# Optimization experiments

Measured on AMD Instinct MI355X. Metric: run time of the kernel, lower is better.

Reference implementation:

```python
import jax, jax.numpy as jnp
import numpy as np

N_EVENTS = 16384   # original pixel events
D = 128            # input_size
H = 128            # hidden_size
K = 9              # kernel 3x3 -> patch coords
S = 2048           # number of patch sequences
LMAX = 108         # max sequence length
T = 147456         # total patch events = sum(lengths) = 9 * N_EVENTS


def setup_inputs() -> dict:
    key = jax.random.key(0)
    ks = jax.random.split(key, 8)
    events = jax.random.normal(ks[0], (N_EVENTS, D), jnp.float32)
    pos_id = jax.random.randint(ks[1], (T,), 0, K, dtype=jnp.int32)
    orig_event_idx = jax.random.randint(ks[2], (T,), 0, N_EVENTS, dtype=jnp.int32)
    # alternating 36/108 lengths: 1024*36 + 1024*108 = 147456 = T
    lengths = jnp.where(jnp.arange(S) % 2 == 0, 36, 108).astype(jnp.int32)
    std = float(np.sqrt(2.0 / (D + H)))
    scatter_w = jax.random.normal(ks[3], (K, H, D), jnp.float32) * std
    gather_w = jax.random.normal(ks[4], (K, H, H), jnp.float32) * std
    lstm_std = float(1.0 / np.sqrt(H))
    w_ih = jax.random.uniform(ks[5], (4 * H, H), jnp.float32, -lstm_std, lstm_std)
    w_hh = jax.random.uniform(ks[6], (4 * H, H), jnp.float32, -lstm_std, lstm_std)
    ln_g = jnp.ones((H,), jnp.float32)
    ln_b = jnp.zeros((H,), jnp.float32)
    return dict(events=events, scatter_w=scatter_w, gather_w=gather_w,
                w_ih=w_ih, w_hh=w_hh, ln_g=ln_g, ln_b=ln_b,
                pos_id=pos_id, orig_event_idx=orig_event_idx, lengths=lengths)


def _pos_proj(x, W, pos_id):
    # position-indexed projection: out[t] = W[pos_id[t]] @ x[t]
    # loop over small fixed K=9 with masked accumulate (matches the torch loop)
    out = jnp.zeros((x.shape[0], W.shape[1]), x.dtype)
    for k in range(W.shape[0]):
        out = out + jnp.where((pos_id == k)[:, None], x @ W[k].T, 0.0)
    return out


def reference(events, scatter_w, gather_w, w_ih, w_hh, ln_g, ln_b,
              pos_id, orig_event_idx, lengths):
    # scatter events to patch replicas
    x = events[orig_event_idx]                           # [T, D]
    x = _pos_proj(x, scatter_w, pos_id)                  # [T, H]

    # flat (sequence-major) -> padded [S, LMAX, H]
    seq_offsets = jnp.cumsum(lengths) - lengths          # [S]
    seq_ids = jnp.repeat(jnp.arange(S), lengths, total_repeat_length=T)
    pos_in_seq = jnp.arange(T) - seq_offsets[seq_ids]
    padded = jnp.zeros((S, LMAX, H), x.dtype).at[seq_ids, pos_in_seq].set(x)

    # single-layer bias-free LSTM (pytorch gate order i, f, g, o), zero init.
    # zero-padding after each sequence's valid region leaves valid outputs
    # identical to a PackedSequence LSTM.
    def step(carry, xt):                                 # xt: [S, H]
        h, c = carry
        gates = xt @ w_ih.T + h @ w_hh.T                 # [S, 4H]
        i, f, g, o = jnp.split(gates, 4, axis=-1)
        c = jax.nn.sigmoid(f) * c + jax.nn.sigmoid(i) * jnp.tanh(g)
        h = jax.nn.sigmoid(o) * jnp.tanh(c)
        return (h, c), h

    init = (jnp.zeros((S, H), x.dtype), jnp.zeros((S, H), x.dtype))
    _, hs = jax.lax.scan(step, init, jnp.swapaxes(padded, 0, 1))  # [LMAX, S, H]
    o_flat = jnp.swapaxes(hs, 0, 1)[seq_ids, pos_in_seq]          # [T, H]

    o_flat = _pos_proj(o_flat, gather_w, pos_id)                  # [T, H]

    # gather patch events back to pixel events (scatter-add) + residual + LN
    out = jnp.zeros((N_EVENTS, H), x.dtype).at[orig_event_idx].add(o_flat)
    out = out + events                                   # input_proj is None (D == H)
    mu = jnp.mean(out, axis=-1, keepdims=True)
    var = jnp.var(out, axis=-1, keepdims=True)
    out = (out - mu) * jax.lax.rsqrt(var + 1e-5) * ln_g + ln_b
    return out
```

## Files before the change

kernel.cpp:

```cpp
#include <hip/hip_runtime.h>

#define N_EVENTS 16384
#define DIM 128
#define NK 9
#define NSEQ 2048
#define TT 147456
#define CHUNK 64
#define NCHUNK_MAX (TT/CHUNK + NK)
#define NHBLK 576

typedef __attribute__((ext_vector_type(8))) short bf16x8;
typedef __attribute__((ext_vector_type(4))) float f32x4;
typedef __attribute__((ext_vector_type(4))) int i32x4;

#define OFF_EV     0UL
#define OFF_WC     (OFF_EV   + (size_t)N_EVENTS*DIM*2)
#define OFF_SCAT   (OFF_WC   + (size_t)512*256*2)
#define OFF_GATH   (OFF_SCAT + (size_t)NK*DIM*DIM*2)
#define OFF_XS     (OFF_GATH + (size_t)NK*DIM*DIM*2)
#define OFF_HS     (OFF_XS   + (size_t)TT*DIM*2)
#define OFF_KLIST  (OFF_HS   + (size_t)TT*DIM*2)
#define OFF_ACC    (OFF_KLIST+ (size_t)TT*4)
#define OFF_SEQOFF (OFF_ACC  + (size_t)N_EVENTS*DIM*4)
#define OFF_GROUP  (OFF_SEQOFF + (size_t)NSEQ*4)
#define OFF_MISC   (OFF_GROUP  + (size_t)NSEQ*4)
#define OFF_BH     (OFF_MISC   + 256UL)

__device__ __forceinline__ short f2b(float f) {
    union { float f; unsigned u; } v; v.f = f;
    unsigned r = (v.u + 0x7FFFu + ((v.u >> 16) & 1u)) >> 16;
    return (short)r;
}

__global__ void convert_kernel(const float* __restrict__ ev, const float* __restrict__ wih,
                               const float* __restrict__ whh, const float* __restrict__ sw,
                               const float* __restrict__ gw,
                               short* __restrict__ evb, short* __restrict__ wcb,
                               short* __restrict__ swb, short* __restrict__ gwb,
                               float* __restrict__ acc) {
    int idx = blockIdx.x * blockDim.x + threadIdx.x;
    if (idx < N_EVENTS * DIM) { evb[idx] = f2b(ev[idx]); acc[idx] = 0.f; }
    if (idx < 512 * DIM) {
        int j = idx >> 7, d = idx & 127;
        wcb[j * 256 + d]       = f2b(wih[idx]);
        wcb[j * 256 + 128 + d] = f2b(whh[idx]);
    }
    if (idx < NK * DIM * DIM) { swb[idx] = f2b(sw[idx]); gwb[idx] = f2b(gw[idx]); }
}

__global__ void hist_kernel(const int* __restrict__ pos, int* __restrict__ blockhist) {
    __shared__ int h[NK];
    int tid = threadIdx.x;
    if (tid < NK) h[tid] = 0;
    __syncthreads();
    atomicAdd(&h[pos[blockIdx.x * 256 + tid]], 1);
    __syncthreads();
    if (tid < NK) blockhist[blockIdx.x * NK + tid] = h[tid];
}

__global__ void scan_kernel(int* __restrict__ blockhist, int* __restrict__ misc) {
    __shared__ int h[NHBLK * NK];
    int tid = threadIdx.x;
    for (int i = tid; i < NHBLK * NK; i += 256) h[i] = blockhist[i];
    __syncthreads();
    if (tid < NK) {
        int run = 0;
        for (int b = 0; b < NHBLK; b++) {
            int v = h[b * NK + tid];
            h[b * NK + tid] = run;
            run += v;
        }
        misc[tid] = run;
    }
    __syncthreads();
    if (tid == 0) {
        int ko = 0, co = 0;
        for (int k = 0; k < NK; k++) {
            int c = misc[k];
            misc[32 + k] = ko;
            misc[48 + k] = co;
            ko += c;
            co += (c + CHUNK - 1) / CHUNK;
        }
        misc[48 + NK] = co;
    }
    __syncthreads();
    for (int i = tid; i < NHBLK * NK; i += 256) blockhist[i] = h[i];
}

__global__ void setup_kernel(const int* __restrict__ lengths,
                             int* __restrict__ seq_off, int* __restrict__ grouped) {
    __shared__ int lens[NSEQ];
    __shared__ int tsum[256], tlong[256];
    int tid = threadIdx.x;
    for (int i = tid; i < NSEQ; i += 256) lens[i] = lengths[i];
    __syncthreads();
    int base = tid * 8;
    int ls[8]; int s = 0, lc = 0;
    #pragma unroll
    for (int i = 0; i < 8; i++) { ls[i] = lens[base + i]; s += ls[i]; lc += (ls[i] > 64) ? 1 : 0; }
    tsum[tid] = s; tlong[tid] = lc;
    __syncthreads();
    for (int d = 1; d < 256; d <<= 1) {
        int a = (tid >= d) ? tsum[tid - d] : 0;
        int b = (tid >= d) ? tlong[tid - d] : 0;
        __syncthreads();
        tsum[tid] += a; tlong[tid] += b;
        __syncthreads();
    }
    int nlong_total = tlong[255];
    int excl = tsum[tid] - s;
    int excl_long = tlong[tid] - lc;
    int run = 0, runl = 0;
    #pragma unroll
    for (int i = 0; i < 8; i++) {
        int sid = base + i;
        seq_off[sid] = excl + run;
        int longs_before = excl_long + runl;
        if (ls[i] > 64) { grouped[longs_before] = sid; runl++; }
        else            { grouped[nlong_total + (sid - longs_before)] = sid; }
        run += ls[i];
    }
}

__global__ void fill2_kernel(const int* __restrict__ pos, const int* __restrict__ blockhist,
                             const int* __restrict__ misc, int* __restrict__ klist) {
    __shared__ int off[NK];
    int tid = threadIdx.x;
    if (tid < NK) off[tid] = misc[32 + tid] + blockhist[blockIdx.x * NK + tid];
    __syncthreads();
    int t = blockIdx.x * 256 + tid;
    int p = atomicAdd(&off[pos[t]], 1);
    klist[p] = t;
}

__global__ void bucket_gemm(const short* __restrict__ src, const short* __restrict__ wall,
                            const int* __restrict__ klist, const int* __restrict__ misc,
                            const int* __restrict__ orig, short* __restrict__ xs_out,
                            float* __restrict__ acc, int mode) {
    const int* chunkoff = misc + 48;
    int b = blockIdx.x;
    if (b >= chunkoff[NK]) return;
    int k = 0;
    while (k < NK - 1 && chunkoff[k + 1] <= b) k++;
    int lc = b - chunkoff[k];
    int cnt = misc[k];
    int base = misc[32 + k] + lc * CHUNK;
    int nv = min(CHUNK, cnt - lc * CHUNK);

    __shared__ int tok[CHUNK], dst[CHUNK];
    __shared__ short A[CHUNK * 136];
    int tid = threadIdx.x;
    if (tid < CHUNK) {
        int tv = klist[base + ((tid < nv) ? tid : 0)];
        tok[tid] = tv;
        dst[tid] = orig[tv];
    }
    __syncthreads();
    {
        int row = tid >> 2, part = tid & 3;
        int ridx = (mode == 0) ? dst[row] : tok[row];
        const i32x4* s4 = (const i32x4*)(src + (size_t)ridx * DIM + part * 32);
        i32x4* d4 = (i32x4*)(A + row * 136 + part * 32);
        d4[0] = s4[0]; d4[1] = s4[1]; d4[2] = s4[2]; d4[3] = s4[3];
    }
    __syncthreads();
    int wave = tid >> 6, lane = tid & 63, l15 = lane & 15, q = lane >> 4;
    const short* wk = wall + (size_t)k * DIM * DIM;
    bf16x8 Bf[2][4];
    #pragma unroll
    for (int nt = 0; nt < 2; nt++) {
        int h = wave * 32 + nt * 16 + l15;
        #pragma unroll
        for (int kt = 0; kt < 4; kt++)
            Bf[nt][kt] = *(const bf16x8*)(wk + h * DIM + kt * 32 + q * 8);
    }
    f32x4 C[4][2];
    #pragma unroll
    for (int mt = 0; mt < 4; mt++)
        #pragma unroll
        for (int nt = 0; nt < 2; nt++) C[mt][nt] = (f32x4){0.f, 0.f, 0.f, 0.f};
    #pragma unroll
    for (int mt = 0; mt < 4; mt++) {
        bf16x8 Afr[4];
        const short* ar = A + (mt * 16 + l15) * 136 + q * 8;
        Afr[0] = *(const bf16x8*)(ar);
        Afr[1] = *(const bf16x8*)(ar + 32);
        Afr[2] = *(const bf16x8*)(ar + 64);
        Afr[3] = *(const bf16x8*)(ar + 96);
        #pragma unroll
        for (int nt = 0; nt < 2; nt++)
            #pragma unroll
            for (int kt = 0; kt < 4; kt++)
                C[mt][nt] = __builtin_amdgcn_mfma_f32_16x16x32_bf16(Afr[kt], Bf[nt][kt], C[mt][nt], 0, 0, 0);
    }
    if (mode == 0) {
        __syncthreads();
        #pragma unroll
        for (int mt = 0; mt < 4; mt++)
            #pragma unroll
            for (int nt = 0; nt < 2; nt++)
                #pragma unroll
                for (int r = 0; r < 4; r++) {
                    int row = mt * 16 + q * 4 + r;
                    int col = wave * 32 + nt * 16 + l15;
                    A[row * 136 + col] = f2b(C[mt][nt][r]);
                }
        __syncthreads();
        int row = tid >> 2, part = tid & 3;
        if (row < nv) {
            const i32x4* s4 = (const i32x4*)(A + row * 136 + part * 32);
            i32x4* d4 = (i32x4*)(xs_out + (size_t)tok[row] * DIM + part * 32);
            d4[0] = s4[0]; d4[1] = s4[1]; d4[2] = s4[2]; d4[3] = s4[3];
        }
    } else {
        #pragma unroll
        for (int mt = 0; mt < 4; mt++)
            #pragma unroll
            for (int nt = 0; nt < 2; nt++)
                #pragma unroll
                for (int r = 0; r < 4; r++) {
                    int row = mt * 16 + q * 4 + r;
                    if (row < nv) {
                        int col = wave * 32 + nt * 16 + l15;
                        atomicAdd(acc + (size_t)dst[row] * DIM + col, C[mt][nt][r]);
                    }
                }
    }
}

#define MF(a, b, c) __builtin_amdgcn_mfma_f32_16x16x32_bf16(a, b, c, 0, 0, 0)

#define LSTM_STEP(J, PF) { \
    const int i_ = ib8 + (J); \
    f32x4 Cxi = {0.f,0.f,0.f,0.f}, Cxf = {0.f,0.f,0.f,0.f}; \
    f32x4 Cxg = {0.f,0.f,0.f,0.f}, Cxo = {0.f,0.f,0.f,0.f}; \
    Cxi = MF(PF[0], Bf[0][0], Cxi); Cxf = MF(PF[0], Bf[1][0], Cxf); \
    Cxg = MF(PF[0], Bf[2][0], Cxg); Cxo = MF(PF[0], Bf[3][0], Cxo); \
    Cxi = MF(PF[1], Bf[0][1], Cxi); Cxf = MF(PF[1], Bf[1][1], Cxf); \
    Cxg = MF(PF[1], Bf[2][1], Cxg); Cxo = MF(PF[1], Bf[3][1], Cxo); \
    Cxi = MF(PF[2], Bf[0][2], Cxi); Cxf = MF(PF[2], Bf[1][2], Cxf); \
    Cxg = MF(PF[2], Bf[2][2], Cxg); Cxo = MF(PF[2], Bf[3][2], Cxo); \
    Cxi = MF(PF[3], Bf[0][3], Cxi); Cxf = MF(PF[3], Bf[1][3], Cxf); \
    Cxg = MF(PF[3], Bf[2][3], Cxg); Cxo = MF(PF[3], Bf[3][3], Cxo); \
    bf16x8 Hf0, Hf1, Hf2, Hf3; \
    { const short* hp_ = hb + (((J) + 7) & 7) * 1088 + l15 * 136 + ql * 8; \
      Hf0 = *(const bf16x8*)(hp_);      Hf1 = *(const bf16x8*)(hp_ + 32); \
      Hf2 = *(const bf16x8*)(hp_ + 64); Hf3 = *(const bf16x8*)(hp_ + 96); } \
    f32x4 Chi = {0.f,0.f,0.f,0.f}, Chf = {0.f,0.f,0.f,0.f}; \
    f32x4 Chg = {0.f,0.f,0.f,0.f}, Cho = {0.f,0.f,0.f,0.f}; \
    Chi = MF(Hf0, Bf[0][4], Chi); Chf = MF(Hf0, Bf[1][4], Chf); \
    Chg = MF(Hf0, Bf[2][4], Chg); Cho = MF(Hf0, Bf[3][4], Cho); \
    Chi = MF(Hf1, Bf[0][5], Chi); Chf = MF(Hf1, Bf[1][5], Chf); \
    Chg = MF(Hf1, Bf[2][5], Chg); Cho = MF(Hf1, Bf[3][5], Cho); \
    Chi = MF(Hf2, Bf[0][6], Chi); Chf = MF(Hf2, Bf[1][6], Chf); \
    Chg = MF(Hf2, Bf[2][6], Chg); Cho = MF(Hf2, Bf[3][6], Cho); \
    Chi = MF(Hf3, Bf[0][7], Chi); Chf = MF(Hf3, Bf[1][7], Chf); \
    Chg = MF(Hf3, Bf[2][7], Chg); Cho = MF(Hf3, Bf[3][7], Cho); \
    if (l15 < 8) { \
        const short* xp_ = xs + xoff; \
        PF[0] = *(const bf16x8*)(xp_);      PF[1] = *(const bf16x8*)(xp_ + 32); \
        PF[2] = *(const bf16x8*)(xp_ + 64); PF[3] = *(const bf16x8*)(xp_ + 96); \
    } \
    xoff += ((i_ + 4) <= my_len) ? DIM : 0; \
    f32x4 Gi = Cxi + Chi, Gf = Cxf + Chf, Gg = Cxg + Chg, Go = Cxo + Cho; \
    { \
        int src_ = lane & 31; \
        float i2 = __shfl(Gi[2], src_, 64), i3 = __shfl(Gi[3], src_, 64); \
        float f2 = __shfl(Gf[2], src_, 64), f3 = __shfl(Gf[3], src_, 64); \
        float g2 = __shfl(Gg[2], src_, 64), g3 = __shfl(Gg[3], src_, 64); \
        float o2 = __shfl(Go[2], src_, 64), o3 = __shfl(Go[3], src_, 64); \
        float iA = lo ? Gi[0] : i2, iB = lo ? Gi[1] : i3; \
        float fA = lo ? Gf[0] : f2, fB = lo ? Gf[1] : f3; \
        float gA = lo ? Gg[0] : g2, gB = lo ? Gg[1] : g3; \
        float oA = lo ? Go[0] : o2, oB = lo ? Go[1] : o3; \
        if (i_ < lenA) { \
            float si = 1.f / (1.f + __expf(-iA)); \
            float sf = 1.f / (1.f + __expf(-fA)); \
            float so = 1.f / (1.f + __expf(-oA)); \
            float tg = 1.f - 2.f / (__expf(2.f * gA) + 1.f); \
            float cn = sf * cA + si * tg; \
            float th = 1.f - 2.f / (__expf(2.f * cn) + 1.f); \
            cA = cn; \
            hb[(J) * 1088 + rowA * 136 + u] = f2b(so * th); \
        } \
        if (i_ < lenB) { \
            float si = 1.f / (1.f + __expf(-iB)); \
            float sf = 1.f / (1.f + __expf(-fB)); \
            float so = 1.f / (1.f + __expf(-oB)); \
            float tg = 1.f - 2.f / (__expf(2.f * gB) + 1.f); \
            float cn = sf * cB + si * tg; \
            float th = 1.f - 2.f / (__expf(2.f * cn) + 1.f); \
            cB = cn; \
            hb[(J) * 1088 + rowB * 136 + u] = f2b(so * th); \
        } \
    } \
    __syncthreads(); \
}

__global__ __launch_bounds__(512, 2) void lstm_kernel(
        const short* __restrict__ xs, const short* __restrict__ wc,
        short* __restrict__ hstore, const int* __restrict__ seq_off,
        const int* __restrict__ grouped, const int* __restrict__ lengths) {
    __shared__ int s_off[8], s_len[8];
    __shared__ short hchunk[11][8][136];
    int tid = threadIdx.x;
    if (tid < 8) {
        int s = grouped[blockIdx.x * 8 + tid];
        s_off[tid] = seq_off[s];
        s_len[tid] = lengths[s];
    }
    for (int j = tid; j < 11 * 8 * 136; j += 512) ((short*)hchunk)[j] = 0;
    __syncthreads();
    int lane = tid & 63, l15 = lane & 15, ql = lane >> 4;
    int wave = tid >> 6;
    int u = wave * 16 + l15;
    short* hb = (short*)hchunk;
    bf16x8 Bf[4][8];
    #pragma unroll
    for (int g = 0; g < 4; g++) {
        int j = g * 128 + u;
        #pragma unroll
        for (int kt = 0; kt < 8; kt++)
            Bf[g][kt] = *(const bf16x8*)(wc + j * 256 + kt * 32 + ql * 8);
    }
    int maxlen = 0;
    #pragma unroll
    for (int i = 0; i < 8; i++) maxlen = max(maxlen, s_len[i]);
    int my_off = (l15 < 8) ? s_off[l15] : 0;
    int my_len = (l15 < 8) ? s_len[l15] : 1;
    bool lo = (ql < 2);
    int rowA = lo ? (ql * 4 + 0) : ((ql - 2) * 4 + 2);
    int rowB = lo ? (ql * 4 + 1) : ((ql - 2) * 4 + 3);
    int lenA = s_len[rowA], lenB = s_len[rowB];
    float cA = 0.f, cB = 0.f;
    bf16x8 Pf0[4], Pf1[4];
    #pragma unroll
    for (int k = 0; k < 4; k++) { Pf0[k] = (bf16x8){0,0,0,0,0,0,0,0}; Pf1[k] = Pf0[k]; }
    int xoff = my_off * DIM + ql * 8;
    if (l15 < 8) {
        const short* xp = xs + xoff;
        Pf0[0] = *(const bf16x8*)(xp);      Pf0[1] = *(const bf16x8*)(xp + 32);
        Pf0[2] = *(const bf16x8*)(xp + 64); Pf0[3] = *(const bf16x8*)(xp + 96);
    }
    int xoff1 = xoff + ((my_len > 1) ? DIM : 0);
    if (l15 < 8) {
        const short* xp = xs + xoff1;
        Pf1[0] = *(const bf16x8*)(xp);      Pf1[1] = *(const bf16x8*)(xp + 32);
        Pf1[2] = *(const bf16x8*)(xp + 64); Pf1[3] = *(const bf16x8*)(xp + 96);
    }
    xoff = xoff1 + ((my_len > 2) ? DIM : 0);

    int nb8 = (maxlen + 7) >> 3;
    for (int ob = 0; ob < nb8; ob++) {
        int ib8 = ob * 8;
        LSTM_STEP(0, Pf0)
        LSTM_STEP(1, Pf1)
        LSTM_STEP(2, Pf0)
        LSTM_STEP(3, Pf1)
        LSTM_STEP(4, Pf0)
        LSTM_STEP(5, Pf1)
        LSTM_STEP(6, Pf0)
        LSTM_STEP(7, Pf1)
        #pragma unroll
        for (int it = 0; it < 2; it++) {
            int idx = tid + it * 512;
            int st = idx >> 7, s = (idx >> 4) & 7, part = idx & 15;
            int ig = ib8 + st;
            if (ig < s_len[s]) {
                i32x4 v = *(const i32x4*)&hchunk[st][s][part * 8];
                *(i32x4*)(hstore + (size_t)(s_off[s] + ig) * DIM + part * 8) = v;
            }
        }
        __syncthreads();
    }
}

__global__ void ln_kernel(const float* __restrict__ acc, const float* __restrict__ events,
                          const float* __restrict__ g, const float* __restrict__ bta,
                          float* __restrict__ out) {
    int tid = threadIdx.x;
    int wave = tid >> 6, lane = tid & 63;
    int e = blockIdx.x * 4 + wave;
    const float2* a2 = (const float2*)(acc + (size_t)e * DIM);
    const float2* e2 = (const float2*)(events + (size_t)e * DIM);
    float2 av = a2[lane], ev = e2[lane];
    float x0 = av.x + ev.x, x1 = av.y + ev.y;
    float sm = x0 + x1, sq = x0 * x0 + x1 * x1;
    #pragma unroll
    for (int m = 1; m < 64; m <<= 1) {
        sm += __shfl_xor(sm, m, 64);
        sq += __shfl_xor(sq, m, 64);
    }
    float mean = sm * (1.f / DIM);
    float var = sq * (1.f / DIM) - mean * mean;
    float rs = rsqrtf(var + 1e-5f);
    float2 gv = ((const float2*)g)[lane], bv = ((const float2*)bta)[lane];
    float2 ov;
    ov.x = (x0 - mean) * rs * gv.x + bv.x;
    ov.y = (x1 - mean) * rs * gv.y + bv.y;
    ((float2*)(out + (size_t)e * DIM))[lane] = ov;
}

extern "C" void kernel_launch(void* const* d_in, const int* in_sizes, int n_in,
                              void* d_out, int out_size, void* d_ws, size_t ws_size,
                              hipStream_t stream) {
    const float* events = (const float*)d_in[0];
    const float* scat   = (const float*)d_in[1];
    const float* gath   = (const float*)d_in[2];
    const float* wih    = (const float*)d_in[3];
    const float* whh    = (const float*)d_in[4];
    const float* lng    = (const float*)d_in[5];
    const float* lnb    = (const float*)d_in[6];
    const int* posid    = (const int*)d_in[7];
    const int* orig     = (const int*)d_in[8];
    const int* lens     = (const int*)d_in[9];
    char* ws = (char*)d_ws;
    short* evb   = (short*)(ws + OFF_EV);
    short* wcb   = (short*)(ws + OFF_WC);
    short* swb   = (short*)(ws + OFF_SCAT);
    short* gwb   = (short*)(ws + OFF_GATH);
    short* xs    = (short*)(ws + OFF_XS);
    short* hs    = (short*)(ws + OFF_HS);
    int*   klist = (int*)(ws + OFF_KLIST);
    float* acc   = (float*)(ws + OFF_ACC);
    int*   seqo  = (int*)(ws + OFF_SEQOFF);
    int*   grp   = (int*)(ws + OFF_GROUP);
    int*   misc  = (int*)(ws + OFF_MISC);
    int*   bh    = (int*)(ws + OFF_BH);
    float* out   = (float*)d_out;

    convert_kernel<<<8192, 256, 0, stream>>>(events, wih, whh, scat, gath, evb, wcb, swb, gwb, acc);
    hist_kernel<<<NHBLK, 256, 0, stream>>>(posid, bh);
    scan_kernel<<<1, 256, 0, stream>>>(bh, misc);
    setup_kernel<<<1, 256, 0, stream>>>(lens, seqo, grp);
    fill2_kernel<<<NHBLK, 256, 0, stream>>>(posid, bh, misc, klist);
    bucket_gemm<<<NCHUNK_MAX, 256, 0, stream>>>(evb, swb, klist, misc, orig, xs, nullptr, 0);
    lstm_kernel<<<256, 512, 0, stream>>>(xs, wcb, hs, seqo, grp, lens);
    bucket_gemm<<<NCHUNK_MAX, 256, 0, stream>>>(hs, gwb, klist, misc, orig, nullptr, acc, 1);
    ln_kernel<<<4096, 256, 0, stream>>>(acc, events, lng, lnb, out);
}
```

Baseline: 347.3 us.

## Stage LSTM input rows into double-buffered LDS window via async global-to-LDS loads

Replaces the per-step register prefetch of x rows, where each lane issued global loads every timestep, with a shared-memory window holding 8 timesteps for 8 sequences. The window is filled by global_load_lds DMA one block of 8 steps ahead, with double buffering. The swizzled layout is meant to avoid bank conflicts on the MFMA operand reads. This takes global-load latency off the recurrent critical path at the cost of 32KB of extra LDS, which may reduce occupancy. It also relies on the existing per-step barriers to order the async LDS writes, with no explicit wait on them.

```diff
diff --git a/kernel.cpp b/kernel.cpp
--- a/kernel.cpp
+++ b/kernel.cpp
@@ -30,6 +30,12 @@
     union { float f; unsigned u; } v; v.f = f;
     unsigned r = (v.u + 0x7FFFu + ((v.u >> 16) & 1u)) >> 16;
     return (short)r;
+}
+
+__device__ __forceinline__ void glds16(const short* gp, short* lp) {
+    __builtin_amdgcn_global_load_lds(
+        (const __attribute__((address_space(1))) void*)gp,
+        (__attribute__((address_space(3))) void*)lp, 16, 0, 0);
 }
 
 __global__ void convert_kernel(const float* __restrict__ ev, const float* __restrict__ wih,
@@ -231,22 +237,27 @@
 
 #define MF(a, b, c) __builtin_amdgcn_mfma_f32_16x16x32_bf16(a, b, c, 0, 0, 0)
 
-#define LSTM_STEP(J, PF) { \
+#define LSTM_STEP(J) { \
     const int i_ = ib8 + (J); \
+    const short* hp_ = hb + (((J) + 7) & 7) * 1088 + l15 * 136 + ql * 8; \
+    bf16x8 Hf0 = *(const bf16x8*)(hp_); \
+    bf16x8 Hf1 = *(const bf16x8*)(hp_ + 32); \
+    bf16x8 Hf2 = *(const bf16x8*)(hp_ + 64); \
+    bf16x8 Hf3 = *(const bf16x8*)(hp_ + 96); \
+    bf16x8 Xf0 = *(const bf16x8*)(vx0 + (J) * 1024); \
+    bf16x8 Xf1 = *(const bf16x8*)(vx1 + (J) * 1024); \
+    bf16x8 Xf2 = *(const bf16x8*)(vx2 + (J) * 1024); \
+    bf16x8 Xf3 = *(const bf16x8*)(vx3 + (J) * 1024); \
     f32x4 Cxi = {0.f,0.f,0.f,0.f}, Cxf = {0.f,0.f,0.f,0.f}; \
     f32x4 Cxg = {0.f,0.f,0.f,0.f}, Cxo = {0.f,0.f,0.f,0.f}; \
-    Cxi = MF(PF[0], Bf[0][0], Cxi); Cxf = MF(PF[0], Bf[1][0], Cxf); \
-    Cxg = MF(PF[0], Bf[2][0], Cxg); Cxo = MF(PF[0], Bf[3][0], Cxo); \
-    Cxi = MF(PF[1], Bf[0][1], Cxi); Cxf = MF(PF[1], Bf[1][1], Cxf); \
-    Cxg = MF(PF[1], Bf[2][1], Cxg); Cxo = MF(PF[1], Bf[3][1], Cxo); \
-    Cxi = MF(PF[2], Bf[0][2], Cxi); Cxf = MF(PF[2], Bf[1][2], Cxf); \
-    Cxg = MF(PF[2], Bf[2][2], Cxg); Cxo = MF(PF[2], Bf[3][2], Cxo); \
-    Cxi = MF(PF[3], Bf[0][3], Cxi); Cxf = MF(PF[3], Bf[1][3], Cxf); \
-    Cxg = MF(PF[3], Bf[2][3], Cxg); Cxo = MF(PF[3], Bf[3][3], Cxo); \
-    bf16x8 Hf0, Hf1, Hf2, Hf3; \
-    { const short* hp_ = hb + (((J) + 7) & 7) * 1088 + l15 * 136 + ql * 8; \
-      Hf0 = *(const bf16x8*)(hp_);      Hf1 = *(const bf16x8*)(hp_ + 32); \
-      Hf2 = *(const bf16x8*)(hp_ + 64); Hf3 = *(const bf16x8*)(hp_ + 96); } \
+    Cxi = MF(Xf0, Bf[0][0], Cxi); Cxf = MF(Xf0, Bf[1][0], Cxf); \
+    Cxg = MF(Xf0, Bf[2][0], Cxg); Cxo = MF(Xf0, Bf[3][0], Cxo); \
+    Cxi = MF(Xf1, Bf[0][1], Cxi); Cxf = MF(Xf1, Bf[1][1], Cxf); \
+    Cxg = MF(Xf1, Bf[2][1], Cxg); Cxo = MF(Xf1, Bf[3][1], Cxo); \
+    Cxi = MF(Xf2, Bf[0][2], Cxi); Cxf = MF(Xf2, Bf[1][2], Cxf); \
+    Cxg = MF(Xf2, Bf[2][2], Cxg); Cxo = MF(Xf2, Bf[3][2], Cxo); \
+    Cxi = MF(Xf3, Bf[0][3], Cxi); Cxf = MF(Xf3, Bf[1][3], Cxf); \
+    Cxg = MF(Xf3, Bf[2][3], Cxg); Cxo = MF(Xf3, Bf[3][3], Cxo); \
     f32x4 Chi = {0.f,0.f,0.f,0.f}, Chf = {0.f,0.f,0.f,0.f}; \
     f32x4 Chg = {0.f,0.f,0.f,0.f}, Cho = {0.f,0.f,0.f,0.f}; \
     Chi = MF(Hf0, Bf[0][4], Chi); Chf = MF(Hf0, Bf[1][4], Chf); \
@@ -257,12 +268,6 @@
     Chg = MF(Hf2, Bf[2][6], Chg); Cho = MF(Hf2, Bf[3][6], Cho); \
     Chi = MF(Hf3, Bf[0][7], Chi); Chf = MF(Hf3, Bf[1][7], Chf); \
     Chg = MF(Hf3, Bf[2][7], Chg); Cho = MF(Hf3, Bf[3][7], Cho); \
-    if (l15 < 8) { \
-        const short* xp_ = xs + xoff; \
-        PF[0] = *(const bf16x8*)(xp_);      PF[1] = *(const bf16x8*)(xp_ + 32); \
-        PF[2] = *(const bf16x8*)(xp_ + 64); PF[3] = *(const bf16x8*)(xp_ + 96); \
-    } \
-    xoff += ((i_ + 4) <= my_len) ? DIM : 0; \
     f32x4 Gi = Cxi + Chi, Gf = Cxf + Chf, Gg = Cxg + Chg, Go = Cxo + Cho; \
     { \
         int src_ = lane & 31; \
@@ -304,6 +309,7 @@
         const int* __restrict__ grouped, const int* __restrict__ lengths) {
     __shared__ int s_off[8], s_len[8];
     __shared__ short hchunk[11][8][136];
+    __shared__ short xwin[2][8][8][128];
     int tid = threadIdx.x;
     if (tid < 8) {
         int s = grouped[blockIdx.x * 8 + tid];
@@ -327,41 +333,56 @@
     int maxlen = 0;
     #pragma unroll
     for (int i = 0; i < 8; i++) maxlen = max(maxlen, s_len[i]);
-    int my_off = (l15 < 8) ? s_off[l15] : 0;
-    int my_len = (l15 < 8) ? s_len[l15] : 1;
     bool lo = (ql < 2);
     int rowA = lo ? (ql * 4 + 0) : ((ql - 2) * 4 + 2);
     int rowB = lo ? (ql * 4 + 1) : ((ql - 2) * 4 + 3);
     int lenA = s_len[rowA], lenB = s_len[rowB];
     float cA = 0.f, cB = 0.f;
-    bf16x8 Pf0[4], Pf1[4];
-    #pragma unroll
-    for (int k = 0; k < 4; k++) { Pf0[k] = (bf16x8){0,0,0,0,0,0,0,0}; Pf1[k] = Pf0[k]; }
-    int xoff = my_off * DIM + ql * 8;
-    if (l15 < 8) {
-        const short* xp = xs + xoff;
-        Pf0[0] = *(const bf16x8*)(xp);      Pf0[1] = *(const bf16x8*)(xp + 32);
-        Pf0[2] = *(const bf16x8*)(xp + 64); Pf0[3] = *(const bf16x8*)(xp + 96);
-    }
-    int xoff1 = xoff + ((my_len > 1) ? DIM : 0);
-    if (l15 < 8) {
-        const short* xp = xs + xoff1;
-        Pf1[0] = *(const bf16x8*)(xp);      Pf1[1] = *(const bf16x8*)(xp + 32);
-        Pf1[2] = *(const bf16x8*)(xp + 64); Pf1[3] = *(const bf16x8*)(xp + 96);
-    }
-    xoff = xoff1 + ((my_len > 2) ? DIM : 0);
+
+    int sg_s0 = lane >> 4;
+    int sg_p  = lane & 15;
+    int sx = l15 & 7;
+    int vxo[4];
+    #pragma unroll
+    for (int i = 0; i < 4; i++)
+        vxo[i] = sx * 128 + (((ql + 4 * i + sx) & 15) * 8);
+
+    #pragma unroll
+    for (int j = 0; j < 2; j++) {
+        int s = j * 4 + sg_s0;
+        int q = (sg_p - s) & 15;
+        int t = s_off[s] + min(wave, s_len[s] - 1);
+        glds16(xs + (size_t)t * DIM + q * 8, &xwin[0][wave][j * 4][0]);
+    }
+    __syncthreads();
 
     int nb8 = (maxlen + 7) >> 3;
     for (int ob = 0; ob < nb8; ob++) {
         int ib8 = ob * 8;
-        LSTM_STEP(0, Pf0)
-        LSTM_STEP(1, Pf1)
-        LSTM_STEP(2, Pf0)
-        LSTM_STEP(3, Pf1)
-        LSTM_STEP(4, Pf0)
-        LSTM_STEP(5, Pf1)
-        LSTM_STEP(6, Pf0)
-        LSTM_STEP(7, Pf1)
+        const short* xw = &xwin[ob & 1][0][0][0];
+        const short* vx0 = xw + vxo[0];
+        const short* vx1 = xw + vxo[1];
+        const short* vx2 = xw + vxo[2];
+        const short* vx3 = xw + vxo[3];
+        if (ob + 1 < nb8) {
+            int gstep = ib8 + 8 + wave;
+            short* lwp = &xwin[(ob + 1) & 1][wave][0][0];
+            #pragma unroll
+            for (int j = 0; j < 2; j++) {
+                int s = j * 4 + sg_s0;
+                int q = (sg_p - s) & 15;
+                int t = s_off[s] + min(gstep, s_len[s] - 1);
+                glds16(xs + (size_t)t * DIM + q * 8, lwp + j * 512);
+            }
+        }
+        LSTM_STEP(0)
+        LSTM_STEP(1)
+        LSTM_STEP(2)
+        LSTM_STEP(3)
+        LSTM_STEP(4)
+        LSTM_STEP(5)
+        LSTM_STEP(6)
+        LSTM_STEP(7)
         #pragma unroll
         for (int it = 0; it < 2; it++) {
             int idx = tid + it * 512;
```

After: 355.3 us. +2.3%, slower.
